# Kernel optimization log

Hardware: AMD Instinct MI355X
Metric: run time of the kernel (lower is better)

Reference implementation:

```python
import jax, jax.numpy as jnp
import numpy as np

D_MODEL = 1024
D_STATE = 256

def setup_inputs() -> dict:
    key = jax.random.key(0)
    k1, k2, k3, k4 = jax.random.split(key, 4)
    x = jax.random.normal(k1, (8, 4096, D_MODEL), dtype=jnp.float32)
    A = jax.random.normal(k2, (D_STATE,), dtype=jnp.float32)
    B = jax.random.normal(k3, (D_STATE, D_MODEL), dtype=jnp.float32) * 0.01
    C = jax.random.normal(k4, (D_MODEL, D_STATE), dtype=jnp.float32) * 0.01
    D = jnp.ones((D_MODEL,), dtype=jnp.float32)
    return {"x": x, "A": A, "B": B, "C": C, "D": D}

def reference(x, A, B, C, D):
    # x: (b, s, d_model)
    a_bar = jnp.exp(-jnp.exp(A))                     # (n,)
    Bx = jnp.einsum('bsd,nd->bsn', x, B)             # (b, s, n) precomputed input drive

    def step(h, bx_t):
        h = a_bar * h + bx_t                          # (b, n)
        return h, h

    h0 = jnp.zeros((x.shape[0], A.shape[0]), dtype=x.dtype)
    # scan over time axis: move seq to leading axis
    _, hs = jax.lax.scan(step, h0, jnp.swapaxes(Bx, 0, 1))  # hs: (s, b, n)
    hs = jnp.swapaxes(hs, 0, 1)                      # (b, s, n)
    y = jnp.einsum('bsn,dn->bsd', hs, C) + D * x     # (b, s, d_model)
    return y
```

## Files before the change

### kernel.cpp

```cpp
#include <hip/hip_runtime.h>
#include <cstdint>
#include <cstddef>


typedef __attribute__((ext_vector_type(8))) _Float16 half8;
typedef __attribute__((ext_vector_type(4))) float f32x4;

__device__ inline half8 cvt8(float4 a, float4 b) {
  half8 h;
  h[0] = (_Float16)a.x; h[1] = (_Float16)a.y;
  h[2] = (_Float16)a.z; h[3] = (_Float16)a.w;
  h[4] = (_Float16)b.x; h[5] = (_Float16)b.y;
  h[6] = (_Float16)b.z; h[7] = (_Float16)b.w;
  return h;
}

__global__ __launch_bounds__(256) void cvt_bc(
    const float* __restrict__ Bp, const float* __restrict__ Cp,
    _Float16* __restrict__ Bh, _Float16* __restrict__ Ch)
{
  const int g = blockIdx.x * 256 + threadIdx.x;
  const size_t off = (size_t)(g & 32767) * 8;
  const float* src = (g < 32768) ? (Bp + off) : (Cp + off);
  _Float16*    dst = (g < 32768) ? (Bh + off) : (Ch + off);
  float4 a = *(const float4*)src;
  float4 b = *(const float4*)(src + 4);
  *(half8*)dst = cvt8(a, b);
}

__global__ __launch_bounds__(256) void gemm_bx(
    const float* __restrict__ x, const _Float16* __restrict__ Bh,
    _Float16* __restrict__ Bxh)
{
  __shared__ _Float16 lb[256 * 128];

  const int tid  = threadIdx.x;
  const int lane = tid & 63;
  const int wave = tid >> 6;
  const int quad = lane >> 4;
  const int l16  = lane & 15;
  const long blockM = (long)blockIdx.x * 64;
  const long arow = blockM + wave * 16 + l16;

  f32x4 acc[16];
  #pragma unroll
  for (int i = 0; i < 16; i++) acc[i] = (f32x4){0.f, 0.f, 0.f, 0.f};

  for (int kc = 0; kc < 8; kc++) {
    __syncthreads();
    {
      const int n = tid;
      const _Float16* src = Bh + (size_t)n * 1024 + kc * 128;
      #pragma unroll
      for (int j = 0; j < 16; j++) {
        half8 v = *(const half8*)(src + j * 8);
        const int k8p = j ^ (n & 7);
        *(half8*)&lb[n * 128 + k8p * 8] = v;
      }
    }
    half8 af[4];
    #pragma unroll
    for (int ks = 0; ks < 4; ks++) {
      const float* ga = x + arow * 1024 + kc * 128 + ks * 32 + quad * 8;
      float4 a0 = *(const float4*)ga;
      float4 a1 = *(const float4*)(ga + 4);
      af[ks] = cvt8(a0, a1);
    }
    __syncthreads();
    #pragma unroll
    for (int ks = 0; ks < 4; ks++) {
      #pragma unroll
      for (int nt = 0; nt < 16; nt++) {
        const int n   = nt * 16 + l16;
        const int k8p = (ks * 4 + quad) ^ (n & 7);
        half8 bf = *(const half8*)&lb[n * 128 + k8p * 8];
        acc[nt] = __builtin_amdgcn_mfma_f32_16x16x32_f16(af[ks], bf, acc[nt], 0, 0, 0);
      }
    }
  }

  __syncthreads();
  #pragma unroll
  for (int nt = 0; nt < 16; nt++)
    #pragma unroll
    for (int r = 0; r < 4; r++)
      lb[(wave * 16 + quad * 4 + r) * 256 + nt * 16 + l16] = (_Float16)acc[nt][r];
  __syncthreads();
  {
    const int row = tid >> 2, seg = tid & 3;
    _Float16* dst = Bxh + (blockM + row) * 256 + seg * 64;
    const _Float16* srcl = &lb[row * 256 + seg * 64];
    #pragma unroll
    for (int j = 0; j < 8; j++)
      *(half8*)(dst + j * 8) = *(const half8*)(srcl + j * 8);
  }
}

__global__ __launch_bounds__(256) void scan_E(
    const _Float16* __restrict__ Bxh, const float* __restrict__ Ap,
    float* __restrict__ E)
{
  const int n  = threadIdx.x;
  const int bc = blockIdx.x;
  const float al = expf(-expf(Ap[n]));
  const size_t base = (size_t)bc * 64 * 256 + n;
  float h = 0.f;
  #pragma unroll 8
  for (int t = 0; t < 64; t++)
    h = fmaf(al, h, (float)Bxh[base + (size_t)t * 256]);
  E[(size_t)bc * 256 + n] = h;
}

__global__ __launch_bounds__(256) void scan_prefix(
    const float* __restrict__ E, const float* __restrict__ Ap,
    float* __restrict__ carry)
{
  const int n = threadIdx.x;
  const int b = blockIdx.x;
  const float al = expf(-expf(Ap[n]));
  float aL = al;
  #pragma unroll
  for (int i = 0; i < 6; i++) aL *= aL;
  float run = 0.f;
  for (int c = 0; c < 64; c++) {
    const size_t idx = ((size_t)b * 64 + c) * 256 + n;
    carry[idx] = run;
    run = fmaf(aL, run, E[idx]);
  }
}

__global__ __launch_bounds__(256) void scan_apply(
    _Float16* __restrict__ Bxh, const float* __restrict__ Ap,
    const float* __restrict__ carry)
{
  const int n  = threadIdx.x;
  const int bc = blockIdx.x;
  const float al = expf(-expf(Ap[n]));
  float h = carry[(size_t)bc * 256 + n];
  const size_t base = (size_t)bc * 64 * 256 + n;
  #pragma unroll 8
  for (int t = 0; t < 64; t++) {
    const size_t i = base + (size_t)t * 256;
    h = fmaf(al, h, (float)Bxh[i]);
    Bxh[i] = (_Float16)h;
  }
}

__global__ __launch_bounds__(256) void gemm_y(
    const _Float16* __restrict__ hs, const _Float16* __restrict__ Ch,
    const float* __restrict__ x, const float* __restrict__ Dp,
    float* __restrict__ y)
{
  __shared__ _Float16 lc[128 * 256];

  const int tid  = threadIdx.x;
  const int lane = tid & 63;
  const int wave = tid >> 6;
  const int quad = lane >> 4;
  const int l16  = lane & 15;
  const int slab = blockIdx.x & 7;
  const int mg   = blockIdx.x >> 3;
  const int n0   = slab * 128;

  {
    const int n = tid >> 1, hf = tid & 1;
    const _Float16* src = Ch + (size_t)(n0 + n) * 256 + hf * 128;
    #pragma unroll
    for (int j = 0; j < 16; j++) {
      half8 v = *(const half8*)(src + j * 8);
      const int k8p = (hf * 16 + j) ^ (n & 7);
      *(half8*)&lc[n * 256 + k8p * 8] = v;
    }
  }

  float dv[8];
  #pragma unroll
  for (int nt = 0; nt < 8; nt++) dv[nt] = Dp[n0 + nt * 16 + l16];

  __syncthreads();

  for (int i = 0; i < 8; i++) {
    const long chunk   = (long)mg * 8 + i;
    const long rowbase = chunk * 64 + wave * 16;

    half8 af[8];
    #pragma unroll
    for (int ks = 0; ks < 8; ks++)
      af[ks] = *(const half8*)(hs + (rowbase + l16) * 256 + ks * 32 + quad * 8);

    float xv[4][8];
    #pragma unroll
    for (int r = 0; r < 4; r++) {
      const float* gx = x + (rowbase + quad * 4 + r) * 1024 + n0 + l16;
      #pragma unroll
      for (int nt = 0; nt < 8; nt++) xv[r][nt] = gx[nt * 16];
    }

    f32x4 acc[8];
    #pragma unroll
    for (int nt = 0; nt < 8; nt++) acc[nt] = (f32x4){0.f, 0.f, 0.f, 0.f};

    #pragma unroll
    for (int ks = 0; ks < 8; ks++) {
      #pragma unroll
      for (int nt = 0; nt < 8; nt++) {
        const int n   = nt * 16 + l16;
        const int k8p = (ks * 4 + quad) ^ (n & 7);
        half8 bf = *(const half8*)&lc[n * 256 + k8p * 8];
        acc[nt] = __builtin_amdgcn_mfma_f32_16x16x32_f16(af[ks], bf, acc[nt], 0, 0, 0);
      }
    }

    #pragma unroll
    for (int r = 0; r < 4; r++) {
      float* gy = y + (rowbase + quad * 4 + r) * 1024 + n0 + l16;
      #pragma unroll
      for (int nt = 0; nt < 8; nt++)
        gy[nt * 16] = acc[nt][r] + dv[nt] * xv[r][nt];
    }
  }
}

extern "C" void kernel_launch(void* const* d_in, const int* in_sizes, int n_in,
                              void* d_out, int out_size, void* d_ws, size_t ws_size,
                              hipStream_t stream) {
  const float* x  = (const float*)d_in[0];
  const float* Ap = (const float*)d_in[1];
  const float* Bp = (const float*)d_in[2];
  const float* Cp = (const float*)d_in[3];
  const float* Dp = (const float*)d_in[4];
  float* y = (float*)d_out;

  _Float16* Bxh = (_Float16*)d_ws;
  _Float16* Bh  = Bxh + (size_t)32768 * 256;
  _Float16* Ch  = Bh + (size_t)256 * 1024;
  float* E      = (float*)(Ch + (size_t)1024 * 256);
  float* carry  = E + (size_t)512 * 256;

  cvt_bc     <<<256, 256, 0, stream>>>(Bp, Cp, Bh, Ch);
  gemm_bx    <<<512, 256, 0, stream>>>(x, Bh, Bxh);
  scan_E     <<<512, 256, 0, stream>>>(Bxh, Ap, E);
  scan_prefix<<<8,   256, 0, stream>>>(E, Ap, carry);
  scan_apply <<<512, 256, 0, stream>>>(Bxh, Ap, carry);
  gemm_y     <<<512, 256, 0, stream>>>(Bxh, Ch, x, Dp, y);
}
```

Measured before the change: 346.7 us.

## Fuse chunk-end scan into Bx GEMM epilogue and retile output GEMM

The per-chunk local scan that produced chunk-end states is folded into the gemm_bx epilogue, reading Bx from LDS instead of re-reading it from global memory. This removes one kernel launch and one full pass over Bx. scan_prefix now stages its E slice in shared memory before the sequential loop. gemm_y is retiled to 64-column slabs with four times as many blocks and a minimum-occupancy hint, which halves its LDS footprint to allow more resident blocks. The cost is more redundant reloads of the fp16 hidden states across slabs in gemm_y.

```diff
diff --git a/kernel.cpp b/kernel.cpp
--- a/kernel.cpp
+++ b/kernel.cpp
@@ -30,7 +30,8 @@
 
 __global__ __launch_bounds__(256) void gemm_bx(
     const float* __restrict__ x, const _Float16* __restrict__ Bh,
-    _Float16* __restrict__ Bxh)
+    const float* __restrict__ Ap,
+    _Float16* __restrict__ Bxh, float* __restrict__ E)
 {
   __shared__ _Float16 lb[256 * 128];
 
@@ -94,38 +95,40 @@
     for (int j = 0; j < 8; j++)
       *(half8*)(dst + j * 8) = *(const half8*)(srcl + j * 8);
   }
-}
-
-__global__ __launch_bounds__(256) void scan_E(
-    const _Float16* __restrict__ Bxh, const float* __restrict__ Ap,
-    float* __restrict__ E)
-{
-  const int n  = threadIdx.x;
-  const int bc = blockIdx.x;
-  const float al = expf(-expf(Ap[n]));
-  const size_t base = (size_t)bc * 64 * 256 + n;
-  float h = 0.f;
-  #pragma unroll 8
-  for (int t = 0; t < 64; t++)
-    h = fmaf(al, h, (float)Bxh[base + (size_t)t * 256]);
-  E[(size_t)bc * 256 + n] = h;
+  {
+    const float al = expf(-expf(Ap[tid]));
+    float h = 0.f;
+    #pragma unroll 8
+    for (int t = 0; t < 64; t++)
+      h = fmaf(al, h, (float)lb[t * 256 + tid]);
+    E[(size_t)blockIdx.x * 256 + tid] = h;
+  }
 }
 
 __global__ __launch_bounds__(256) void scan_prefix(
     const float* __restrict__ E, const float* __restrict__ Ap,
     float* __restrict__ carry)
 {
+  __shared__ float4 se4[4096];
   const int n = threadIdx.x;
   const int b = blockIdx.x;
+
+  const float4* src4 = (const float4*)(E + (size_t)b * 64 * 256);
+  #pragma unroll
+  for (int j = 0; j < 16; j++)
+    se4[j * 256 + n] = src4[j * 256 + n];
+
   const float al = expf(-expf(Ap[n]));
   float aL = al;
   #pragma unroll
   for (int i = 0; i < 6; i++) aL *= aL;
+
+  __syncthreads();
+  const float* se = (const float*)se4;
   float run = 0.f;
   for (int c = 0; c < 64; c++) {
-    const size_t idx = ((size_t)b * 64 + c) * 256 + n;
-    carry[idx] = run;
-    run = fmaf(aL, run, E[idx]);
+    carry[((size_t)b * 64 + c) * 256 + n] = run;
+    run = fmaf(aL, run, se[c * 256 + n]);
   }
 }
 
@@ -138,7 +141,7 @@
   const float al = expf(-expf(Ap[n]));
   float h = carry[(size_t)bc * 256 + n];
   const size_t base = (size_t)bc * 64 * 256 + n;
-  #pragma unroll 8
+  #pragma unroll 16
   for (int t = 0; t < 64; t++) {
     const size_t i = base + (size_t)t * 256;
     h = fmaf(al, h, (float)Bxh[i]);
@@ -146,41 +149,41 @@
   }
 }
 
-__global__ __launch_bounds__(256) void gemm_y(
+__global__ __launch_bounds__(256, 4) void gemm_y(
     const _Float16* __restrict__ hs, const _Float16* __restrict__ Ch,
     const float* __restrict__ x, const float* __restrict__ Dp,
     float* __restrict__ y)
 {
-  __shared__ _Float16 lc[128 * 256];
+  __shared__ _Float16 lc[64 * 256];
 
   const int tid  = threadIdx.x;
   const int lane = tid & 63;
   const int wave = tid >> 6;
   const int quad = lane >> 4;
   const int l16  = lane & 15;
-  const int slab = blockIdx.x & 7;
-  const int mg   = blockIdx.x >> 3;
-  const int n0   = slab * 128;
+  const int slab = blockIdx.x & 15;
+  const int mg   = blockIdx.x >> 4;
+  const int n0   = slab * 64;
 
   {
-    const int n = tid >> 1, hf = tid & 1;
-    const _Float16* src = Ch + (size_t)(n0 + n) * 256 + hf * 128;
-    #pragma unroll
-    for (int j = 0; j < 16; j++) {
+    const int n = tid >> 2, q = tid & 3;
+    const _Float16* src = Ch + (size_t)(n0 + n) * 256 + q * 64;
+    #pragma unroll
+    for (int j = 0; j < 8; j++) {
       half8 v = *(const half8*)(src + j * 8);
-      const int k8p = (hf * 16 + j) ^ (n & 7);
+      const int k8p = (q * 8 + j) ^ (n & 7);
       *(half8*)&lc[n * 256 + k8p * 8] = v;
     }
   }
 
-  float dv[8];
-  #pragma unroll
-  for (int nt = 0; nt < 8; nt++) dv[nt] = Dp[n0 + nt * 16 + l16];
-
-  __syncthreads();
-
-  for (int i = 0; i < 8; i++) {
-    const long chunk   = (long)mg * 8 + i;
+  float dv[4];
+  #pragma unroll
+  for (int nt = 0; nt < 4; nt++) dv[nt] = Dp[n0 + nt * 16 + l16];
+
+  __syncthreads();
+
+  for (int i = 0; i < 4; i++) {
+    const long chunk   = (long)mg * 4 + i;
     const long rowbase = chunk * 64 + wave * 16;
 
     half8 af[8];
@@ -188,22 +191,22 @@
     for (int ks = 0; ks < 8; ks++)
       af[ks] = *(const half8*)(hs + (rowbase + l16) * 256 + ks * 32 + quad * 8);
 
-    float xv[4][8];
+    float xv[4][4];
     #pragma unroll
     for (int r = 0; r < 4; r++) {
       const float* gx = x + (rowbase + quad * 4 + r) * 1024 + n0 + l16;
       #pragma unroll
-      for (int nt = 0; nt < 8; nt++) xv[r][nt] = gx[nt * 16];
-    }
-
-    f32x4 acc[8];
-    #pragma unroll
-    for (int nt = 0; nt < 8; nt++) acc[nt] = (f32x4){0.f, 0.f, 0.f, 0.f};
+      for (int nt = 0; nt < 4; nt++) xv[r][nt] = gx[nt * 16];
+    }
+
+    f32x4 acc[4];
+    #pragma unroll
+    for (int nt = 0; nt < 4; nt++) acc[nt] = (f32x4){0.f, 0.f, 0.f, 0.f};
 
     #pragma unroll
     for (int ks = 0; ks < 8; ks++) {
       #pragma unroll
-      for (int nt = 0; nt < 8; nt++) {
+      for (int nt = 0; nt < 4; nt++) {
         const int n   = nt * 16 + l16;
         const int k8p = (ks * 4 + quad) ^ (n & 7);
         half8 bf = *(const half8*)&lc[n * 256 + k8p * 8];
@@ -215,7 +218,7 @@
     for (int r = 0; r < 4; r++) {
       float* gy = y + (rowbase + quad * 4 + r) * 1024 + n0 + l16;
       #pragma unroll
-      for (int nt = 0; nt < 8; nt++)
+      for (int nt = 0; nt < 4; nt++)
         gy[nt * 16] = acc[nt][r] + dv[nt] * xv[r][nt];
     }
   }
@@ -237,10 +240,9 @@
   float* E      = (float*)(Ch + (size_t)1024 * 256);
   float* carry  = E + (size_t)512 * 256;
 
-  cvt_bc     <<<256, 256, 0, stream>>>(Bp, Cp, Bh, Ch);
-  gemm_bx    <<<512, 256, 0, stream>>>(x, Bh, Bxh);
-  scan_E     <<<512, 256, 0, stream>>>(Bxh, Ap, E);
-  scan_prefix<<<8,   256, 0, stream>>>(E, Ap, carry);
-  scan_apply <<<512, 256, 0, stream>>>(Bxh, Ap, carry);
-  gemm_y     <<<512, 256, 0, stream>>>(Bxh, Ch, x, Dp, y);
-}
+  cvt_bc     <<<256,  256, 0, stream>>>(Bp, Cp, Bh, Ch);
+  gemm_bx    <<<512,  256, 0, stream>>>(x, Bh, Ap, Bxh, E);
+  scan_prefix<<<8,    256, 0, stream>>>(E, Ap, carry);
+  scan_apply <<<512,  256, 0, stream>>>(Bxh, Ap, carry);
+  gemm_y     <<<2048, 256, 0, stream>>>(Bxh, Ch, x, Dp, y);
+}
```

New measurement: 334.6 us. 3.5% less time.
